# Kernel tuning notes

Measured on AMD Instinct MI355X. Metric: run time of the kernel, lower is better.

## Reference

```python
import jax, jax.numpy as jnp
import numpy as np

N = 50000      # nodes
E = 800000     # random edges (self loops appended in reference)
B = 500        # graphs
H = 4          # attention heads
F = 64         # feature_dim (per-head out channels)
SLOPE = 0.2    # GATConv leaky_relu negative slope


def gat_layer(x, src, dst, W, att_s, att_d, b):
    # x: [N, Fin]; W: [Fin, H*F]; att_s/att_d: [H, F]; b: [H*F]
    h = (x @ W).reshape(N, H, F)                       # [N,H,F]
    a_s = jnp.einsum('nhf,hf->nh', h, att_s)           # [N,H]
    a_d = jnp.einsum('nhf,hf->nh', h, att_d)           # [N,H]
    e = jax.nn.leaky_relu(a_s[src] + a_d[dst], SLOPE)  # [E',H]
    emax = jax.ops.segment_max(e, dst, num_segments=N) # [N,H] (finite: self loops)
    ee = jnp.exp(e - emax[dst])
    denom = jax.ops.segment_sum(ee, dst, num_segments=N)
    alpha = ee / denom[dst]                            # [E',H]
    out = jax.ops.segment_sum(alpha[:, :, None] * h[src], dst, num_segments=N)
    return out.reshape(N, H * F) + b


def setup_inputs() -> dict:
    key = jax.random.key(0)
    ks = jax.random.split(key, 32)
    s = 0.05
    inp = {
        'node_features': jax.random.normal(ks[0], (N, 5), jnp.float32),
        'building_mask': jax.random.randint(ks[1], (N,), 0, 2),
        'batch': jnp.sort(jax.random.randint(ks[2], (N,), 0, B)),
        'edge_index': jax.random.randint(ks[3], (2, E), 0, N),
        'bbox_W': jax.random.normal(ks[4], (5, 64)) * s,
        'bbox_b': jnp.zeros((64,), jnp.float32),
        'mask_embed': jax.random.normal(ks[5], (2, 64)) * s,
        'node_W': jax.random.normal(ks[6], (128, 64)) * s,
        'node_b': jnp.zeros((64,), jnp.float32),
        'w0': jax.random.normal(ks[7], (64, 256)) * s,
        'as0': jax.random.normal(ks[8], (H, F)) * s,
        'ad0': jax.random.normal(ks[9], (H, F)) * s,
        'b0': jnp.zeros((256,), jnp.float32),
        'w1': jax.random.normal(ks[10], (256, 256)) * s,
        'as1': jax.random.normal(ks[11], (H, F)) * s,
        'ad1': jax.random.normal(ks[12], (H, F)) * s,
        'b1': jnp.zeros((256,), jnp.float32),
        'w2': jax.random.normal(ks[13], (256, 256)) * s,
        'as2': jax.random.normal(ks[14], (H, F)) * s,
        'ad2': jax.random.normal(ks[15], (H, F)) * s,
        'b2': jnp.zeros((256,), jnp.float32),
        'agg_W': jax.random.normal(ks[16], (832, 256)) * s,
        'agg_b': jnp.zeros((256,), jnp.float32),
        'mu_W': jax.random.normal(ks[17], (256, 256)) * s,
        'mu_b': jnp.zeros((256,), jnp.float32),
        'var_W': jax.random.normal(ks[18], (256, 256)) * s,
        'var_b': jnp.zeros((256,), jnp.float32),
    }
    return inp


def reference(node_features, building_mask, batch, edge_index,
              bbox_W, bbox_b, mask_embed, node_W, node_b,
              w0, as0, ad0, b0, w1, as1, ad1, b1, w2, as2, ad2, b2,
              agg_W, agg_b, mu_W, mu_b, var_W, var_b):
    # node featurization
    x = jax.nn.relu(node_features @ bbox_W + bbox_b)          # [N,64]
    m = jax.nn.relu(mask_embed[building_mask])                 # [N,64]
    n0 = jax.nn.relu(jnp.concatenate([x, m], -1) @ node_W + node_b)  # [N,64]

    # self loops (GATConv add_self_loops=True)
    loop = jnp.arange(N, dtype=edge_index.dtype)
    src = jnp.concatenate([edge_index[0], loop])
    dst = jnp.concatenate([edge_index[1], loop])

    g = jax.ops.segment_max(n0, batch, num_segments=B, indices_are_sorted=True)
    g_embed = [g]

    n_t = jax.nn.relu(gat_layer(n0, src, dst, w0, as0, ad0, b0))
    g_embed.append(jax.ops.segment_max(n_t, batch, num_segments=B, indices_are_sorted=True))

    for (W, a_s, a_d, b) in [(w1, as1, ad1, b1), (w2, as2, ad2, b2)]:
        n_t = jax.nn.relu(gat_layer(n_t, src, dst, W, a_s, a_d, b))
        g_embed.append(jax.ops.segment_max(n_t, batch, num_segments=B, indices_are_sorted=True))

    latent = jnp.concatenate(g_embed, -1) @ agg_W + agg_b      # [B,256]
    mu = latent @ mu_W + mu_b
    log_var = latent @ var_W + var_b
    return (mu, log_var)
```

## Files before the change

### kernel.cpp

```cpp
#include <hip/hip_runtime.h>

#define NN 50000
#define EE 800000
#define BB 500
#define SCB 196

typedef short v8s __attribute__((ext_vector_type(8)));
typedef float v4f __attribute__((ext_vector_type(4)));

__device__ __forceinline__ float bf2f(unsigned short u) {
    union { unsigned int i; float f; } v; v.i = ((unsigned int)u) << 16; return v.f;
}
__device__ __forceinline__ unsigned short f2bf(float f) {
    union { float f; unsigned int i; } v; v.f = f;
    unsigned int x = v.i;
    unsigned int r = (x + 0x7FFFu + ((x >> 16) & 1u)) >> 16;
    return (unsigned short)r;
}

__global__ void k_sentinel(float* out, float val) {
    int i = blockIdx.x * blockDim.x + threadIdx.x;
    if (i < BB * 512) out[i] = val;
}

__global__ void k_prep(const float* __restrict__ nf, const int* __restrict__ bmask,
                       const float* __restrict__ bboxW, const float* __restrict__ bboxb,
                       const float* __restrict__ membed, unsigned short* __restrict__ feat,
                       const float* __restrict__ a0, unsigned short* __restrict__ d0,
                       const float* __restrict__ a1, unsigned short* __restrict__ d1,
                       const float* __restrict__ a2, unsigned short* __restrict__ d2,
                       const float* __restrict__ a3, unsigned short* __restrict__ d3,
                       int* __restrict__ counts) {
    int g = blockIdx.x * blockDim.x + threadIdx.x;
    if (g < NN) counts[g] = 1;
    if (g < NN * 64) {
        int n = g >> 6, f = g & 63;
        float s = bboxb[f];
        for (int k = 0; k < 5; ++k) s += nf[n * 5 + k] * bboxW[k * 64 + f];
        s = fmaxf(s, 0.f);
        int bm = bmask[n]; if ((unsigned)bm > 1u) bm = 0;
        float mv = fmaxf(membed[bm * 64 + f], 0.f);
        feat[(size_t)n * 128 + f] = f2bf(s);
        feat[(size_t)n * 128 + 64 + f] = f2bf(mv);
        return;
    }
    g -= NN * 64;
    const float* in; unsigned short* out; int K, Nout, idx;
    if (g < 8192)        { in = a0; out = d0; K = 128; Nout = 64;  idx = g; }
    else if (g < 24576)  { in = a1; out = d1; K = 64;  Nout = 256; idx = g - 8192; }
    else if (g < 90112)  { in = a2; out = d2; K = 256; Nout = 256; idx = g - 24576; }
    else if (g < 155648) { in = a3; out = d3; K = 256; Nout = 256; idx = g - 90112; }
    else return;
    int k = idx / Nout, n = idx % Nout;
    out[n * K + k] = f2bf(in[idx]);
}

template <int KT, bool BR, bool ATT>
__global__ __launch_bounds__(256) void k_gemm(const unsigned short* __restrict__ A,
                                              const unsigned short* __restrict__ Bt,
                                              const float* __restrict__ bias,
                                              unsigned short* __restrict__ C, int M, int ldc,
                                              const float* __restrict__ atts, const float* __restrict__ attd,
                                              float* __restrict__ asA, float* __restrict__ adA) {
    constexpr int NT = KT / 64;
    constexpr int NB = (NT > 1) ? 2 : 1;
    __shared__ v8s As[NB][64 * 8];
    __shared__ v8s Bs[NB][64 * 8];
    __shared__ float ap[4][4][4][4][2];
    const int t = threadIdx.x;
    const int m0 = blockIdx.x * 64;
    const int n0 = blockIdx.y * 64;
    const int l = t & 63, w = t >> 6;
    const int q = l >> 4, r16 = l & 15;
    const int nloc = w * 16 + r16;

    const int sm = t >> 3, kcl = t & 7;
    const int swz = kcl ^ (sm & 7);
    const int arow0 = m0 + sm, arow1 = m0 + sm + 32;
    const unsigned short* Bp0 = Bt + (size_t)(n0 + sm) * KT + kcl * 8;
    const unsigned short* Bp1 = Bt + (size_t)(n0 + sm + 32) * KT + kcl * 8;
    const unsigned short* Ap0 = A + (size_t)arow0 * KT + kcl * 8;
    const unsigned short* Ap1 = A + (size_t)arow1 * KT + kcl * 8;

    v8s ra0, ra1, rb0, rb1;
    const v8s vz = (v8s){0, 0, 0, 0, 0, 0, 0, 0};
    auto loadT = [&](int kt) {
        ra0 = (arow0 < M) ? *(const v8s*)(Ap0 + kt * 64) : vz;
        ra1 = (arow1 < M) ? *(const v8s*)(Ap1 + kt * 64) : vz;
        rb0 = *(const v8s*)(Bp0 + kt * 64);
        rb1 = *(const v8s*)(Bp1 + kt * 64);
    };
    auto storeT = [&](int b) {
        As[b][sm * 8 + swz] = ra0;
        As[b][(sm + 32) * 8 + swz] = ra1;
        Bs[b][sm * 8 + swz] = rb0;
        Bs[b][(sm + 32) * 8 + swz] = rb1;
    };

    v4f acc[4];
#pragma unroll
    for (int i = 0; i < 4; ++i) acc[i] = (v4f){0.f, 0.f, 0.f, 0.f};

    loadT(0);
    storeT(0);
    __syncthreads();
#pragma unroll
    for (int kt = 0; kt < NT; ++kt) {
        const int b = kt & (NB - 1);
        if (kt + 1 < NT) loadT(kt + 1);
#pragma unroll
        for (int s = 0; s < 2; ++s) {
            int c = s * 4 + q;
            v8s bfr = Bs[b][nloc * 8 + (c ^ (nloc & 7))];
#pragma unroll
            for (int mt = 0; mt < 4; ++mt) {
                v8s afr = As[b][(mt * 16 + r16) * 8 + (c ^ (r16 & 7))];
                acc[mt] = __builtin_amdgcn_mfma_f32_16x16x32_bf16(afr, bfr, acc[mt], 0, 0, 0);
            }
        }
        if (kt + 1 < NT) storeT((kt + 1) & (NB - 1));
        __syncthreads();
    }

    const int col = n0 + nloc;
#pragma unroll
    for (int mt = 0; mt < 4; ++mt) {
#pragma unroll
        for (int r = 0; r < 4; ++r) {
            int row = m0 + mt * 16 + q * 4 + r;
            if (row < M) {
                float v = acc[mt][r];
                if (BR) v = fmaxf(v + bias[col], 0.f);
                C[(size_t)row * ldc + col] = f2bf(v);
            }
        }
    }
    if (ATT) {
        float sa = atts[blockIdx.y * 64 + nloc];
        float da = attd[blockIdx.y * 64 + nloc];
        float rs[4][4], rd[4][4];
#pragma unroll
        for (int mt = 0; mt < 4; ++mt)
#pragma unroll
            for (int r = 0; r < 4; ++r) { rs[mt][r] = acc[mt][r] * sa; rd[mt][r] = acc[mt][r] * da; }
#pragma unroll
        for (int d = 1; d < 16; d <<= 1) {
#pragma unroll
            for (int mt = 0; mt < 4; ++mt)
#pragma unroll
                for (int r = 0; r < 4; ++r) {
                    rs[mt][r] += __shfl_xor(rs[mt][r], d, 64);
                    rd[mt][r] += __shfl_xor(rd[mt][r], d, 64);
                }
        }
        if (r16 == 0) {
#pragma unroll
            for (int mt = 0; mt < 4; ++mt)
#pragma unroll
                for (int r = 0; r < 4; ++r) { ap[w][q][mt][r][0] = rs[mt][r]; ap[w][q][mt][r][1] = rd[mt][r]; }
        }
        __syncthreads();
        if (t < 128) {
            int row = t >> 1, which = t & 1;
            int qq = (row >> 2) & 3, mtt = row >> 4, rr = row & 3;
            float s = ap[0][qq][mtt][rr][which] + ap[1][qq][mtt][rr][which] +
                      ap[2][qq][mtt][rr][which] + ap[3][qq][mtt][rr][which];
            if (m0 + row < M) (which ? adA : asA)[(m0 + row) * 4 + blockIdx.y] = s;
        }
    }
}

__global__ void k_count(const int* __restrict__ dst, int* __restrict__ counts) {
    int e = blockIdx.x * blockDim.x + threadIdx.x;
    if (e < EE) {
        int d = dst[e];
        if ((unsigned)d < (unsigned)NN) atomicAdd(&counts[d], 1);
    }
}

__global__ __launch_bounds__(256) void k_scanA(const int* __restrict__ counts, int* __restrict__ bsum) {
    __shared__ int red[256];
    const int b = blockIdx.x, t = threadIdx.x;
    int i = b * 256 + t;
    red[t] = (i < NN) ? counts[i] : 0;
    __syncthreads();
    for (int d = 128; d > 0; d >>= 1) {
        if (t < d) red[t] += red[t + d];
        __syncthreads();
    }
    if (t == 0) bsum[b] = red[0];
}

__global__ __launch_bounds__(256) void k_scanB(const int* __restrict__ bsum, int* __restrict__ boff) {
    __shared__ int s[256];
    const int t = threadIdx.x;
    int v = (t < SCB) ? bsum[t] : 0;
    s[t] = v;
    __syncthreads();
    for (int d = 1; d < 256; d <<= 1) {
        int x = (t >= d) ? s[t - d] : 0;
        __syncthreads();
        s[t] += x;
        __syncthreads();
    }
    if (t < SCB) boff[t] = s[t] - v;
}

__global__ __launch_bounds__(256) void k_scanC(const int* __restrict__ counts, const int* __restrict__ boff,
                                               int* __restrict__ off, int* __restrict__ cur) {
    __shared__ int s[256];
    const int b = blockIdx.x, t = threadIdx.x;
    int i = b * 256 + t;
    int v = (i < NN) ? counts[i] : 0;
    s[t] = v;
    __syncthreads();
    for (int d = 1; d < 256; d <<= 1) {
        int x = (t >= d) ? s[t - d] : 0;
        __syncthreads();
        s[t] += x;
        __syncthreads();
    }
    int excl = s[t] - v + boff[b];
    if (i < NN) { off[i] = excl; cur[i] = excl; }
    if (i == NN - 1) off[NN] = excl + v;
}

#define SCAT_K 256
__global__ __launch_bounds__(256) void k_scatter(const int* __restrict__ ei, int* __restrict__ cur,
                                                 int* __restrict__ csr) {
    const int p = blockIdx.x & 7;
    const int j = blockIdx.x >> 3;
    const int plo = p * (NN / 8), phi = plo + (NN / 8);
    const int TOT = EE + NN;
    const int chunk = (TOT + SCAT_K - 1) / SCAT_K;
    const int e1 = min((j + 1) * chunk, TOT);
    for (int e = j * chunk + (int)threadIdx.x; e < e1; e += 256) {
        int d = (e < EE) ? ei[EE + e] : (e - EE);
        if (d < plo || d >= phi) continue;
        int s = (e < EE) ? ei[e] : d;
        if ((unsigned)s >= (unsigned)NN) s = d;
        int pos = atomicAdd(&cur[d], 1);
        csr[pos] = s;
    }
}

__global__ __launch_bounds__(256) void k_agg(const unsigned short* __restrict__ h,
                                             const float* __restrict__ asA, const float* __restrict__ adA,
                                             const int* __restrict__ off, const int* __restrict__ csr,
                                             const float* __restrict__ bias,
                                             unsigned short* __restrict__ nout, int base) {
    __shared__ int   sL[4][64];
    __shared__ float wL[4][64][4];
    const int nd4 = threadIdx.x >> 6;
    const int node = base + blockIdx.x * 4 + nd4;
    const int l = threadIdx.x & 63;
    const int hl = l >> 4, k16 = l & 15;
    const int o0 = off[node];
    const int deg = off[node + 1] - o0;
    const int dcap = deg < 64 ? deg : 64;
    const float ad4 = adA[node * 4 + hl];
    float sm = 0.f;
    for (int k = k16; k < dcap; k += 16) {
        int s = csr[o0 + k];
        if (hl == 0) sL[nd4][k] = s;
        float e = asA[s * 4 + hl] + ad4;
        e = e > 0.f ? e : 0.2f * e;
        float w = __expf(e);
        wL[nd4][k][hl] = w;
        sm += w;
    }
    for (int k = 64 + k16; k < deg; k += 16) {
        int s = csr[o0 + k];
        float e = asA[s * 4 + hl] + ad4;
        e = e > 0.f ? e : 0.2f * e;
        sm += __expf(e);
    }
#pragma unroll
    for (int d = 1; d < 16; d <<= 1) sm += __shfl_xor(sm, d, 64);
    const float rden = 1.f / sm;
    __syncthreads();
    float a0 = 0.f, a1 = 0.f, a2 = 0.f, a3 = 0.f;
    const int c = l * 4;
    int k = 0;
    for (; k + 4 <= dcap; k += 4) {
        int s0 = sL[nd4][k], s1 = sL[nd4][k + 1], s2 = sL[nd4][k + 2], s3 = sL[nd4][k + 3];
        float w0 = wL[nd4][k][hl], w1 = wL[nd4][k + 1][hl], w2 = wL[nd4][k + 2][hl], w3 = wL[nd4][k + 3][hl];
        ushort4 h0 = *(const ushort4*)(h + (size_t)s0 * 256 + c);
        ushort4 h1 = *(const ushort4*)(h + (size_t)s1 * 256 + c);
        ushort4 h2 = *(const ushort4*)(h + (size_t)s2 * 256 + c);
        ushort4 h3 = *(const ushort4*)(h + (size_t)s3 * 256 + c);
        a0 += w0 * bf2f(h0.x) + w1 * bf2f(h1.x) + w2 * bf2f(h2.x) + w3 * bf2f(h3.x);
        a1 += w0 * bf2f(h0.y) + w1 * bf2f(h1.y) + w2 * bf2f(h2.y) + w3 * bf2f(h3.y);
        a2 += w0 * bf2f(h0.z) + w1 * bf2f(h1.z) + w2 * bf2f(h2.z) + w3 * bf2f(h3.z);
        a3 += w0 * bf2f(h0.w) + w1 * bf2f(h1.w) + w2 * bf2f(h2.w) + w3 * bf2f(h3.w);
    }
    for (; k < dcap; ++k) {
        int s = sL[nd4][k];
        float w = wL[nd4][k][hl];
        ushort4 hv = *(const ushort4*)(h + (size_t)s * 256 + c);
        a0 += w * bf2f(hv.x); a1 += w * bf2f(hv.y); a2 += w * bf2f(hv.z); a3 += w * bf2f(hv.w);
    }
    for (int k2 = 64; k2 < deg; ++k2) {
        int s = csr[o0 + k2];
        float e = asA[s * 4 + hl] + ad4;
        e = e > 0.f ? e : 0.2f * e;
        float w = __expf(e);
        ushort4 hv = *(const ushort4*)(h + (size_t)s * 256 + c);
        a0 += w * bf2f(hv.x); a1 += w * bf2f(hv.y); a2 += w * bf2f(hv.z); a3 += w * bf2f(hv.w);
    }
    float4 bv = *(const float4*)(bias + c);
    ushort4 o;
    o.x = f2bf(fmaxf(a0 * rden + bv.x, 0.f));
    o.y = f2bf(fmaxf(a1 * rden + bv.y, 0.f));
    o.z = f2bf(fmaxf(a2 * rden + bv.z, 0.f));
    o.w = f2bf(fmaxf(a3 * rden + bv.w, 0.f));
    *(ushort4*)(nout + (size_t)node * 256 + c) = o;
}

__global__ __launch_bounds__(256) void k_gmaxseg(const unsigned short* __restrict__ nt, int cols,
                                                 const int* __restrict__ batch,
                                                 float* __restrict__ gcat, int gbase) {
    __shared__ float red[256];
    const int b = blockIdx.x, t = threadIdx.x;
    const int lane = t & 63, chunk = t >> 6;
    const int c = blockIdx.y * 64 + lane;
    int lo = 0, hi = NN;
    while (lo < hi) { int mid = (lo + hi) >> 1; if (batch[mid] < b) lo = mid + 1; else hi = mid; }
    int lo2 = lo, hi2 = NN;
    while (lo2 < hi2) { int mid = (lo2 + hi2) >> 1; if (batch[mid] < b + 1) lo2 = mid + 1; else hi2 = mid; }
    float m = 0.f;
    for (int n = lo + chunk; n < lo2; n += 4)
        m = fmaxf(m, bf2f(nt[(size_t)n * cols + c]));
    red[t] = m;
    __syncthreads();
    if (chunk == 0) {
        m = fmaxf(fmaxf(m, red[64 + lane]), fmaxf(red[128 + lane], red[192 + lane]));
        gcat[b * 832 + gbase + c] = m;
    }
}

__global__ __launch_bounds__(256) void k_final(const float* __restrict__ gcat,
                                               const float* __restrict__ aggW, const float* __restrict__ aggb,
                                               const float* __restrict__ muW, const float* __restrict__ mub,
                                               const float* __restrict__ vaW, const float* __restrict__ vab,
                                               float* __restrict__ out) {
    __shared__ float gr[832];
    __shared__ float lat[256];
    const int b = blockIdx.x, t = threadIdx.x;
    for (int i = t; i < 832; i += 256) gr[i] = gcat[b * 832 + i];
    __syncthreads();
    float s0 = 0.f, s1 = 0.f, s2 = 0.f, s3 = 0.f;
#pragma unroll 4
    for (int k = 0; k < 832; k += 4) {
        s0 += gr[k + 0] * aggW[(k + 0) * 256 + t];
        s1 += gr[k + 1] * aggW[(k + 1) * 256 + t];
        s2 += gr[k + 2] * aggW[(k + 2) * 256 + t];
        s3 += gr[k + 3] * aggW[(k + 3) * 256 + t];
    }
    lat[t] = ((s0 + s1) + (s2 + s3)) + aggb[t];
    __syncthreads();
    float m0 = 0.f, m1 = 0.f, v0 = 0.f, v1 = 0.f;
#pragma unroll 4
    for (int k = 0; k < 256; k += 2) {
        float l0 = lat[k], l1 = lat[k + 1];
        m0 += l0 * muW[(k + 0) * 256 + t];
        m1 += l1 * muW[(k + 1) * 256 + t];
        v0 += l0 * vaW[(k + 0) * 256 + t];
        v1 += l1 * vaW[(k + 1) * 256 + t];
    }
    out[b * 256 + t] = (m0 + m1) + mub[t];
    out[BB * 256 + b * 256 + t] = (v0 + v1) + vab[t];
}

extern "C" void kernel_launch(void* const* d_in, const int* in_sizes, int n_in,
                              void* d_out, int out_size, void* d_ws, size_t ws_size,
                              hipStream_t stream) {
    (void)in_sizes; (void)n_in; (void)out_size;
    const float* nf     = (const float*)d_in[0];
    const int*   bmask  = (const int*)d_in[1];
    const int*   batch  = (const int*)d_in[2];
    const int*   ei     = (const int*)d_in[3];
    const float* bboxW  = (const float*)d_in[4];
    const float* bboxb  = (const float*)d_in[5];
    const float* membed = (const float*)d_in[6];
    const float* nodeW  = (const float*)d_in[7];
    const float* nodeb  = (const float*)d_in[8];
    const float* w0     = (const float*)d_in[9];
    const float* as0    = (const float*)d_in[10];
    const float* ad0    = (const float*)d_in[11];
    const float* b0     = (const float*)d_in[12];
    const float* w1     = (const float*)d_in[13];
    const float* as1    = (const float*)d_in[14];
    const float* ad1    = (const float*)d_in[15];
    const float* b1     = (const float*)d_in[16];
    const float* w2     = (const float*)d_in[17];
    const float* as2    = (const float*)d_in[18];
    const float* ad2    = (const float*)d_in[19];
    const float* b2     = (const float*)d_in[20];
    const float* aggW   = (const float*)d_in[21];
    const float* aggb   = (const float*)d_in[22];
    const float* muW    = (const float*)d_in[23];
    const float* mub    = (const float*)d_in[24];
    const float* vaW    = (const float*)d_in[25];
    const float* vab    = (const float*)d_in[26];
    float* out = (float*)d_out;

    char* base = (char*)d_ws;
    unsigned short* hbuf    = (unsigned short*)(base);
    unsigned short* nbuf    = (unsigned short*)(base + 25600000);
    unsigned short* feat128 = nbuf;
    unsigned short* n0buf   = (unsigned short*)(base + 25600000 + 12800000);
    char* pool0 = base + 51200000;
    char* p = pool0;
    auto alloc = [&](size_t bytes) { char* r = p; p += (bytes + 255) & ~(size_t)255; return r; };
    unsigned short* nodeWt = (unsigned short*)alloc(128 * 64 * 2);
    unsigned short* w0t    = (unsigned short*)alloc(64 * 256 * 2);
    unsigned short* w1t    = (unsigned short*)alloc(256 * 256 * 2);
    unsigned short* w2t    = (unsigned short*)alloc(256 * 256 * 2);
    float* asA    = (float*)alloc((size_t)NN * 4 * 4);
    float* adA    = (float*)alloc((size_t)NN * 4 * 4);
    int*   counts = (int*)alloc((size_t)NN * 4);
    int*   offs   = (int*)alloc((size_t)(NN + 1) * 4);
    int*   cur    = (int*)alloc((size_t)NN * 4);
    int*   csr    = (int*)alloc((size_t)(EE + NN) * 4);
    float* gcat   = (float*)alloc((size_t)BB * 832 * 4);
    int*   bsum   = (int*)alloc(SCB * 4);
    int*   boff   = (int*)alloc(SCB * 4);
    const size_t NEED = (size_t)(p - base);

    if (ws_size < NEED) {
        k_sentinel<<<1000, 256, 0, stream>>>(out, 2000.0f + (float)(ws_size >> 20));
        return;
    }

    k_prep<<<(NN * 64 + 155648 + 255) / 256, 256, 0, stream>>>(nf, bmask, bboxW, bboxb, membed, feat128,
                                                               nodeW, nodeWt, w0, w0t, w1, w1t, w2, w2t, counts);
    k_count<<<(EE + 255) / 256, 256, 0, stream>>>(ei + EE, counts);
    k_scanA<<<SCB, 256, 0, stream>>>(counts, bsum);
    k_scanB<<<1, 256, 0, stream>>>(bsum, boff);
    k_scanC<<<SCB, 256, 0, stream>>>(counts, boff, offs, cur);
    k_scatter<<<SCAT_K * 8, 256, 0, stream>>>(ei, cur, csr);
    k_gemm<128, true, false><<<dim3(782, 1), 256, 0, stream>>>(feat128, nodeWt, nodeb, n0buf, NN, 64,
                                                               nullptr, nullptr, nullptr, nullptr);
    k_gmaxseg<<<dim3(BB, 1), 256, 0, stream>>>(n0buf, 64, batch, gcat, 0);
    k_gemm<64, false, true><<<dim3(782, 4), 256, 0, stream>>>(n0buf, w0t, nullptr, hbuf, NN, 256,
                                                              as0, ad0, asA, adA);
    k_agg<<<6250, 256, 0, stream>>>(hbuf, asA, adA, offs, csr, b0, nbuf, 0);
    k_agg<<<6250, 256, 0, stream>>>(hbuf, asA, adA, offs, csr, b0, nbuf, 25000);
    k_gmaxseg<<<dim3(BB, 4), 256, 0, stream>>>(nbuf, 256, batch, gcat, 64);
    k_gemm<256, false, true><<<dim3(782, 4), 256, 0, stream>>>(nbuf, w1t, nullptr, hbuf, NN, 256,
                                                               as1, ad1, asA, adA);
    k_agg<<<6250, 256, 0, stream>>>(hbuf, asA, adA, offs, csr, b1, nbuf, 0);
    k_agg<<<6250, 256, 0, stream>>>(hbuf, asA, adA, offs, csr, b1, nbuf, 25000);
    k_gmaxseg<<<dim3(BB, 4), 256, 0, stream>>>(nbuf, 256, batch, gcat, 320);
    k_gemm<256, false, true><<<dim3(782, 4), 256, 0, stream>>>(nbuf, w2t, nullptr, hbuf, NN, 256,
                                                               as2, ad2, asA, adA);
    k_agg<<<6250, 256, 0, stream>>>(hbuf, asA, adA, offs, csr, b2, nbuf, 0);
    k_agg<<<6250, 256, 0, stream>>>(hbuf, asA, adA, offs, csr, b2, nbuf, 25000);
    k_gmaxseg<<<dim3(BB, 4), 256, 0, stream>>>(nbuf, 256, batch, gcat, 576);
    k_final<<<BB, 256, 0, stream>>>(gcat, aggW, aggb, muW, mub, vaW, vab, out);
}
```

Before: 613.5 us.

## Split final MLP head into two tiled kernels reusing weights across four graphs

Replaces the single per-graph final kernel with two kernels. Each block now handles four graphs and 64 output columns, so every weight load is reused across four graphs and the K dimension is split across warps with a shared-memory reduction. This cuts redundant weight reads from global memory and exposes more parallelism. In exchange it adds an extra launch and an intermediate latent buffer round trip.

```diff
diff --git a/kernel.cpp b/kernel.cpp
--- a/kernel.cpp
+++ b/kernel.cpp
@@ -339,37 +339,70 @@
     }
 }
 
-__global__ __launch_bounds__(256) void k_final(const float* __restrict__ gcat,
+__global__ __launch_bounds__(256) void k_head1(const float* __restrict__ gcat,
                                                const float* __restrict__ aggW, const float* __restrict__ aggb,
+                                               float* __restrict__ latent) {
+    __shared__ float gr[832 * 4];
+    __shared__ float part[4][4][64];
+    const int t = threadIdx.x;
+    const int g0 = blockIdx.x * 4, c0 = blockIdx.y * 64;
+    for (int i = t; i < 832 * 4; i += 256) {
+        int k = i >> 2, g = i & 3;
+        gr[i] = gcat[(g0 + g) * 832 + k];
+    }
+    __syncthreads();
+    const int w = t >> 6, l = t & 63;
+    const float* wp = aggW + c0 + l;
+    float a0 = 0.f, a1 = 0.f, a2 = 0.f, a3 = 0.f;
+    const int k0 = w * 208;
+#pragma unroll 4
+    for (int k = k0; k < k0 + 208; ++k) {
+        float wv = wp[(size_t)k * 256];
+        float4 gv = *(const float4*)&gr[k * 4];
+        a0 += gv.x * wv; a1 += gv.y * wv; a2 += gv.z * wv; a3 += gv.w * wv;
+    }
+    part[w][0][l] = a0; part[w][1][l] = a1; part[w][2][l] = a2; part[w][3][l] = a3;
+    __syncthreads();
+    const int g = t >> 6, c = t & 63;
+    float s = ((part[0][g][c] + part[1][g][c]) + (part[2][g][c] + part[3][g][c])) + aggb[c0 + c];
+    latent[(g0 + g) * 256 + c0 + c] = s;
+}
+
+__global__ __launch_bounds__(256) void k_head2(const float* __restrict__ latent,
                                                const float* __restrict__ muW, const float* __restrict__ mub,
                                                const float* __restrict__ vaW, const float* __restrict__ vab,
                                                float* __restrict__ out) {
-    __shared__ float gr[832];
-    __shared__ float lat[256];
-    const int b = blockIdx.x, t = threadIdx.x;
-    for (int i = t; i < 832; i += 256) gr[i] = gcat[b * 832 + i];
-    __syncthreads();
-    float s0 = 0.f, s1 = 0.f, s2 = 0.f, s3 = 0.f;
+    __shared__ float lr[256 * 4];
+    __shared__ float pm[4][4][64], pv[4][4][64];
+    const int t = threadIdx.x;
+    const int g0 = blockIdx.x * 4, c0 = blockIdx.y * 64;
+    for (int i = t; i < 256 * 4; i += 256) {
+        int k = i >> 2, g = i & 3;
+        lr[i] = latent[(g0 + g) * 256 + k];
+    }
+    __syncthreads();
+    const int w = t >> 6, l = t & 63;
+    const float* mp = muW + c0 + l;
+    const float* vp = vaW + c0 + l;
+    float m0 = 0.f, m1 = 0.f, m2 = 0.f, m3 = 0.f;
+    float v0 = 0.f, v1 = 0.f, v2 = 0.f, v3 = 0.f;
+    const int k0 = w * 64;
 #pragma unroll 4
-    for (int k = 0; k < 832; k += 4) {
-        s0 += gr[k + 0] * aggW[(k + 0) * 256 + t];
-        s1 += gr[k + 1] * aggW[(k + 1) * 256 + t];
-        s2 += gr[k + 2] * aggW[(k + 2) * 256 + t];
-        s3 += gr[k + 3] * aggW[(k + 3) * 256 + t];
-    }
-    lat[t] = ((s0 + s1) + (s2 + s3)) + aggb[t];
-    __syncthreads();
-    float m0 = 0.f, m1 = 0.f, v0 = 0.f, v1 = 0.f;
-#pragma unroll 4
-    for (int k = 0; k < 256; k += 2) {
-        float l0 = lat[k], l1 = lat[k + 1];
-        m0 += l0 * muW[(k + 0) * 256 + t];
-        m1 += l1 * muW[(k + 1) * 256 + t];
-        v0 += l0 * vaW[(k + 0) * 256 + t];
-        v1 += l1 * vaW[(k + 1) * 256 + t];
-    }
-    out[b * 256 + t] = (m0 + m1) + mub[t];
-    out[BB * 256 + b * 256 + t] = (v0 + v1) + vab[t];
+    for (int k = k0; k < k0 + 64; ++k) {
+        float wm = mp[(size_t)k * 256];
+        float wv = vp[(size_t)k * 256];
+        float4 gv = *(const float4*)&lr[k * 4];
+        m0 += gv.x * wm; m1 += gv.y * wm; m2 += gv.z * wm; m3 += gv.w * wm;
+        v0 += gv.x * wv; v1 += gv.y * wv; v2 += gv.z * wv; v3 += gv.w * wv;
+    }
+    pm[w][0][l] = m0; pm[w][1][l] = m1; pm[w][2][l] = m2; pm[w][3][l] = m3;
+    pv[w][0][l] = v0; pv[w][1][l] = v1; pv[w][2][l] = v2; pv[w][3][l] = v3;
+    __syncthreads();
+    const int g = t >> 6, c = t & 63;
+    float smu = ((pm[0][g][c] + pm[1][g][c]) + (pm[2][g][c] + pm[3][g][c])) + mub[c0 + c];
+    float sva = ((pv[0][g][c] + pv[1][g][c]) + (pv[2][g][c] + pv[3][g][c])) + vab[c0 + c];
+    out[(g0 + g) * 256 + c0 + c] = smu;
+    out[BB * 256 + (g0 + g) * 256 + c0 + c] = sva;
 }
 
 extern "C" void kernel_launch(void* const* d_in, const int* in_sizes, int n_in,
@@ -424,6 +457,7 @@
     int*   cur    = (int*)alloc((size_t)NN * 4);
     int*   csr    = (int*)alloc((size_t)(EE + NN) * 4);
     float* gcat   = (float*)alloc((size_t)BB * 832 * 4);
+    float* latent = (float*)alloc((size_t)BB * 256 * 4);
     int*   bsum   = (int*)alloc(SCB * 4);
     int*   boff   = (int*)alloc(SCB * 4);
     const size_t NEED = (size_t)(p - base);
@@ -458,5 +492,6 @@
     k_agg<<<6250, 256, 0, stream>>>(hbuf, asA, adA, offs, csr, b2, nbuf, 0);
     k_agg<<<6250, 256, 0, stream>>>(hbuf, asA, adA, offs, csr, b2, nbuf, 25000);
     k_gmaxseg<<<dim3(BB, 4), 256, 0, stream>>>(nbuf, 256, batch, gcat, 576);
-    k_final<<<BB, 256, 0, stream>>>(gcat, aggW, aggb, muW, mub, vaW, vab, out);
-}
+    k_head1<<<dim3(BB / 4, 4), 256, 0, stream>>>(gcat, aggW, aggb, latent);
+    k_head2<<<dim3(BB / 4, 4), 256, 0, stream>>>(latent, muW, mub, vaW, vab, out);
+}
```

After: 607.6 us. No clear change (-1.0%).
